# Performance work log

Measured on AMD Instinct MI355X. Metric: run time of the kernel, lower is better.

Reference implementation:

```python
import jax, jax.numpy as jnp
import numpy as np

B, DIM, H, W = 2, 384, 256, 256
HID = DIM * 1          # ffn_expansion_factor = 1 (required for source code to be consistent)
P = 8                  # patch_size


def setup_inputs() -> dict:
    key = jax.random.key(0)
    k0, k1, k2, k3, k4 = jax.random.split(key, 5)
    x = jax.random.normal(k0, (B, DIM, H, W), jnp.float32)
    # learned spectral filter: (hidden, P, P//2+1), real-valued, multiplies rfft2 coeffs
    fft_filter = jax.random.normal(k1, (HID, P, P // 2 + 1), jnp.float32)
    # project_in: 1x1 conv dim->hidden, weight (out,in)
    w_in = jax.random.normal(k2, (HID, DIM), jnp.float32) * (1.0 / np.sqrt(DIM))
    # depthwise 3x3 conv, groups=channels, weight (C,1,3,3)
    w_dw = jax.random.normal(k3, (HID, 1, 3, 3), jnp.float32) * (1.0 / 3.0)
    # project_out: 1x1 conv hidden//2 -> dim
    w_out = jax.random.normal(k4, (DIM, HID // 2), jnp.float32) * (1.0 / np.sqrt(HID // 2))
    return {"x": x, "fft_filter": fft_filter, "w_in": w_in, "w_dw": w_dw, "w_out": w_out}


def reference(x, fft_filter, w_in, w_dw, w_out):
    b, c, h, w = x.shape
    hid = w_in.shape[0]
    hb, wb = h // P, w // P
    # project_in (1x1 conv == channel GEMM)
    t = jnp.einsum('bchw,oc->bohw', x, w_in)
    # patchify into 8x8 blocks and apply per-patch 2D real FFT spectral filter.
    # reshape b c (hb p1) (wb p2) -> b c hb p1 wb p2; FFT over axes (3,5).
    tp = t.reshape(b, hid, hb, P, wb, P)
    tf = jnp.fft.rfft2(tp, axes=(3, 5))                 # (b,hid,hb,P,wb,P//2+1) complex
    tf = tf * fft_filter[None, :, None, :, None, :]
    tp = jnp.fft.irfft2(tf, s=(P, P), axes=(3, 5))
    t = tp.reshape(b, hid, h, w)
    # depthwise 3x3 conv, stride 1, padding 1
    t = jax.lax.conv_general_dilated(
        t, w_dw, window_strides=(1, 1), padding='SAME',
        feature_group_count=hid,
        dimension_numbers=('NCHW', 'OIHW', 'NCHW'))
    # gated GELU (exact erf gelu, matching torch F.gelu default)
    x1, x2 = t[:, : hid // 2], t[:, hid // 2:]
    g = jax.nn.gelu(x1, approximate=False) * x2
    # project_out (1x1 conv)
    return jnp.einsum('bchw,oc->bohw', g, w_out)
```

## Files before the change

kernel.cpp:

```cpp
#include <hip/hip_runtime.h>
#include <hip/hip_bf16.h>
#include <math.h>

#define BB 2
#define DIM 384
#define HID 384
#define HW 65536

typedef short s16x8 __attribute__((ext_vector_type(8)));
typedef short s16x4 __attribute__((ext_vector_type(4)));
typedef __bf16 bf16x8 __attribute__((ext_vector_type(8)));
typedef float f32x4 __attribute__((ext_vector_type(4)));

__device__ inline short f2b(float f) {
    __hip_bfloat16 h = __float2bfloat16(f);
    return __builtin_bit_cast(short, h);
}
__device__ inline float b2f(short s) {
    return __bfloat162float(__builtin_bit_cast(__hip_bfloat16, s));
}

__device__ inline void gl_lds16(const short* g, short* l) {
    __builtin_amdgcn_global_load_lds(
        (const __attribute__((address_space(1))) unsigned int*)g,
        (__attribute__((address_space(3))) unsigned int*)l, 16, 0, 0);
}

__global__ void k_prep(const float* __restrict__ w_in, const float* __restrict__ w_out,
                       const float* __restrict__ F,
                       short* __restrict__ wbin, short* __restrict__ wbout,
                       float* __restrict__ Dt, short* __restrict__ Rb) {
    int i = blockIdx.x * 256 + threadIdx.x;
    if (i < 147456) { wbin[i] = f2b(w_in[i]); return; }
    i -= 147456;
    if (i < 73728) { wbout[i] = f2b(w_out[i]); return; }
    i -= 73728;
    if (i < 24576) {
        int c = i >> 6, j = i & 63;
        int a = j >> 3, q = j & 7;
        float d;
        if (q >= 1 && q <= 3)
            d = F[c * 40 + a * 5 + q];
        else if (q >= 5)
            d = F[c * 40 + ((8 - a) & 7) * 5 + (8 - q)];
        else
            d = 0.5f * (F[c * 40 + a * 5 + q] + F[c * 40 + ((8 - a) & 7) * 5 + q]);
        Dt[j * 384 + c] = d * (1.f / 64.f);
        return;
    }
    i -= 24576;
    if (i < 4096) {
        int j = i >> 6, k = i & 63;
        const float cas[8] = {1.f, 1.41421356237f, 1.f, 0.f, -1.f, -1.41421356237f, -1.f, 0.f};
        int t = ((j >> 3) * (k >> 3) + (j & 7) * (k & 7)) & 7;
        Rb[i] = f2b(cas[t]);
    }
}

__global__ __launch_bounds__(256) void k_cvtx(const float* __restrict__ X, short* __restrict__ Xt) {
    int hw0 = blockIdx.x * 64, c0 = blockIdx.y * 64, b = blockIdx.z;
    __shared__ __align__(16) short S[64 * 64];
    int t = threadIdx.x;
    const float* Xb = X + ((size_t)(b * DIM) << 16);
    short* Xtb = Xt + (size_t)b * HW * DIM;
#pragma unroll
    for (int p = 0; p < 2; ++p) {
        int row = p * 32 + (t >> 3), sb = t & 7;
        const float* src = &Xb[((size_t)(c0 + row) << 16) + hw0 + sb * 8];
        float4 a = *(const float4*)src;
        float4 bq = *(const float4*)(src + 4);
        s16x8 v;
        v[0] = f2b(a.x);  v[1] = f2b(a.y);  v[2] = f2b(a.z);  v[3] = f2b(a.w);
        v[4] = f2b(bq.x); v[5] = f2b(bq.y); v[6] = f2b(bq.z); v[7] = f2b(bq.w);
        *(s16x8*)&S[row * 64 + ((sb ^ (row >> 3)) << 3)] = v;
    }
    __syncthreads();
#pragma unroll
    for (int p = 0; p < 2; ++p) {
        int row = p * 32 + (t >> 3), ch = t & 7;
        s16x8 v;
#pragma unroll
        for (int j = 0; j < 8; ++j)
            v[j] = S[(ch * 8 + j) * 64 + (row ^ (ch << 3))];
        *(s16x8*)&Xtb[(size_t)(hw0 + row) * DIM + c0 + ch * 8] = v;
    }
}

__global__ __launch_bounds__(256) void k_gemm1c(const short* __restrict__ A,
                                                const short* __restrict__ Bt,
                                                const short* __restrict__ Rb,
                                                const float* __restrict__ Dt,
                                                short* __restrict__ T) {
    __shared__ __align__(16) short SH[17408 + 4096];
    short* As = SH;
    short* Bs = SH + 4096;
    short* Rs = SH + 17408;
    int d = blockIdx.x;
    int wg = (d & 7) * 192 + (d >> 3);
    int m0 = (wg % 3) * 128;
    int tx = wg / 3;
    int h0 = (tx >> 4) * 8;
    int w0 = (tx & 15) * 16;
    int b  = blockIdx.z;
    const short* Bz = Bt + (size_t)b * HW * DIM;
    int tid = threadIdx.x;
    int lane = tid & 63, w = tid >> 6;
    int wr = w >> 1, wc = w & 1;
    int lm = lane & 15, quad = lane >> 4;

    {
        int j0 = tid >> 3, kb0 = tid & 7;
        gl_lds16(Rb + j0 * 64 + ((kb0 ^ (j0 & 7)) << 3), Rs + tid * 8);
        int t2 = tid + 256;
        int j1 = t2 >> 3, kb1 = t2 & 7;
        gl_lds16(Rb + j1 * 64 + ((kb1 ^ (j1 & 7)) << 3), Rs + t2 * 8);
    }

    f32x4 acc[4][4];
#pragma unroll
    for (int i = 0; i < 4; ++i)
#pragma unroll
        for (int j = 0; j < 4; ++j) acc[i][j] = 0.f;

    int srow = tid >> 2, sseg = tid & 3;
    int pu = srow >> 3, pv = srow & 7;
    int p1 = ((h0 + pu) << 8) + w0 + pv;
    int p2 = p1 + 8;
    for (int k0 = 0; k0 < DIM; k0 += 32) {
        gl_lds16(A + (size_t)(m0 + srow) * DIM + k0 + sseg * 8, As + tid * 8);
        gl_lds16(A + (size_t)(m0 + 64 + srow) * DIM + k0 + sseg * 8, As + (tid + 256) * 8);
        gl_lds16(Bz + (size_t)p1 * DIM + k0 + sseg * 8, Bs + tid * 8);
        gl_lds16(Bz + (size_t)p2 * DIM + k0 + sseg * 8, Bs + (tid + 256) * 8);
        __syncthreads();
        bf16x8 af[4], bfr[4];
#pragma unroll
        for (int i = 0; i < 4; ++i)
            af[i] = __builtin_bit_cast(bf16x8, *(const s16x8*)&As[(wr * 64 + i * 16 + lm) * 32 + quad * 8]);
#pragma unroll
        for (int j = 0; j < 4; ++j)
            bfr[j] = __builtin_bit_cast(bf16x8, *(const s16x8*)&Bs[(wc * 64 + j * 16 + lm) * 32 + quad * 8]);
#pragma unroll
        for (int i = 0; i < 4; ++i)
#pragma unroll
            for (int j = 0; j < 4; ++j)
                acc[i][j] = __builtin_amdgcn_mfma_f32_16x16x32_bf16(af[i], bfr[j], acc[i][j], 0, 0, 0);
        __syncthreads();
    }
#pragma unroll
    for (int i = 0; i < 4; ++i)
#pragma unroll
        for (int j = 0; j < 4; ++j)
#pragma unroll
            for (int r = 0; r < 4; ++r)
                SH[(wr * 64 + i * 16 + quad * 4 + r) * 136 + wc * 64 + j * 16 + lm] =
                    f2b(acc[i][j][r]);

    f32x4 acc2[4][4];
#pragma unroll
    for (int i = 0; i < 4; ++i)
#pragma unroll
        for (int j = 0; j < 4; ++j) acc2[i][j] = 0.f;
#pragma unroll
    for (int ks = 0; ks < 2; ++ks) {
        bf16x8 af[4], bfr[4];
#pragma unroll
        for (int i = 0; i < 4; ++i)
            af[i] = __builtin_bit_cast(bf16x8,
                *(const s16x8*)&SH[(wr * 64 + i * 16 + lm) * 136 + wc * 64 + ks * 32 + quad * 8]);
#pragma unroll
        for (int jf = 0; jf < 4; ++jf)
            bfr[jf] = __builtin_bit_cast(bf16x8,
                *(const s16x8*)&Rs[(jf * 16 + lm) * 64 + (((ks * 4 + quad) ^ (lm & 7)) << 3)]);
#pragma unroll
        for (int i = 0; i < 4; ++i)
#pragma unroll
            for (int jf = 0; jf < 4; ++jf)
                acc2[i][jf] = __builtin_amdgcn_mfma_f32_16x16x32_bf16(af[i], bfr[jf], acc2[i][jf], 0, 0, 0);
    }
#pragma unroll
    for (int i = 0; i < 4; ++i)
#pragma unroll
        for (int jf = 0; jf < 4; ++jf) {
            int j = jf * 16 + lm;
            float4 dv = *(const float4*)&Dt[j * 384 + m0 + wr * 64 + i * 16 + quad * 4];
            acc2[i][jf][0] *= dv.x; acc2[i][jf][1] *= dv.y;
            acc2[i][jf][2] *= dv.z; acc2[i][jf][3] *= dv.w;
        }
#pragma unroll
    for (int i = 0; i < 4; ++i)
#pragma unroll
        for (int jf = 0; jf < 4; ++jf)
#pragma unroll
            for (int r = 0; r < 4; ++r)
                SH[(wr * 64 + i * 16 + quad * 4 + r) * 136 + wc * 64 + jf * 16 + lm] =
                    f2b(acc2[i][jf][r]);

    f32x4 acc3[4][4];
#pragma unroll
    for (int i = 0; i < 4; ++i)
#pragma unroll
        for (int j = 0; j < 4; ++j) acc3[i][j] = 0.f;
#pragma unroll
    for (int ks = 0; ks < 2; ++ks) {
        bf16x8 af[4], bfr[4];
#pragma unroll
        for (int i = 0; i < 4; ++i)
            af[i] = __builtin_bit_cast(bf16x8,
                *(const s16x8*)&SH[(wr * 64 + i * 16 + lm) * 136 + wc * 64 + ks * 32 + quad * 8]);
#pragma unroll
        for (int uf = 0; uf < 4; ++uf)
            bfr[uf] = __builtin_bit_cast(bf16x8,
                *(const s16x8*)&Rs[(uf * 16 + lm) * 64 + (((ks * 4 + quad) ^ (lm & 7)) << 3)]);
#pragma unroll
        for (int i = 0; i < 4; ++i)
#pragma unroll
            for (int uf = 0; uf < 4; ++uf)
                acc3[i][uf] = __builtin_amdgcn_mfma_f32_16x16x32_bf16(af[i], bfr[uf], acc3[i][uf], 0, 0, 0);
    }
#pragma unroll
    for (int i = 0; i < 4; ++i)
#pragma unroll
        for (int uf = 0; uf < 4; ++uf)
#pragma unroll
            for (int r = 0; r < 4; ++r)
                SH[(wr * 64 + i * 16 + quad * 4 + r) * 136 + wc * 64 + uf * 16 + lm] =
                    f2b(acc3[i][uf][r]);
    __syncthreads();
    int pid0 = (h0 >> 3) * 32 + (w0 >> 3);
#pragma unroll
    for (int kq = 0; kq < 8; ++kq) {
        int idx = kq * 256 + tid;
        int row = idx >> 4, seg = idx & 15;
        s16x8 vv = *(const s16x8*)&SH[row * 136 + seg * 8];
        *(s16x8*)&T[(((size_t)(b * HID + m0 + row)) << 16) + (pid0 << 6) + seg * 8] = vv;
    }
}

__global__ __launch_bounds__(256) void k_dwgt(const short* __restrict__ Y,
                                              const float* __restrict__ Wdw,
                                              short* __restrict__ Gt) {
    int bz = blockIdx.z;
    int b  = bz / 24;
    int cg = bz % 24;
    int c0 = cg * 8;
    int h0 = blockIdx.y * 16, w0 = blockIdx.x * 64;
    __shared__ __align__(16) short S[16][18][80];
    __shared__ float sw[16][9];
    int tid = threadIdx.x;
    if (tid < 144) {
        int p = tid / 9, j = tid % 9;
        int ch = (p < 8) ? (c0 + p) : (c0 + p - 8 + 192);
        sw[p][j] = Wdw[ch * 9 + j];
    }
    for (int t = tid; t < 2880; t += 256) {
        int v = t % 10, r = (t / 10) % 18, p = t / 180;
        int gh = h0 + r - 1;
        int gw = w0 + v * 8 - 8;
        int ch = (p < 8) ? (c0 + p) : (c0 + p - 8 + 192);
        s16x8 val = {0, 0, 0, 0, 0, 0, 0, 0};
        if (gh >= 0 && gh < 256 && gw >= 0 && gw <= 248) {
            int pid = ((gh >> 3) << 5) + (gw >> 3);
            val = *(const s16x8*)&Y[((size_t)(b * HID + ch) << 16) + (pid << 6) + ((gh & 7) << 3)];
        }
        *(s16x8*)&S[p][r][v * 8] = val;
    }
    __syncthreads();
    s16x8 ov[4];
#pragma unroll
    for (int it = 0; it < 4; ++it) {
        int idx = it * 256 + tid;
        int p = idx >> 7, run = idx & 127;
        int r = run >> 3, c8 = (run & 7) * 8;
        float z1[8], z2[8];
#pragma unroll
        for (int k = 0; k < 8; ++k) { z1[k] = 0.f; z2[k] = 0.f; }
#pragma unroll
        for (int i = 0; i < 3; ++i) {
            {
                s16x4 wv[4];
#pragma unroll
                for (int q = 0; q < 4; ++q) wv[q] = *(const s16x4*)&S[p][r + i][c8 + 4 + q * 4];
                float fv[10];
#pragma unroll
                for (int q = 0; q < 10; ++q) fv[q] = b2f(wv[(q + 3) >> 2][(q + 3) & 3]);
#pragma unroll
                for (int j = 0; j < 3; ++j) {
                    float wgt = sw[p][i * 3 + j];
#pragma unroll
                    for (int k = 0; k < 8; ++k) z1[k] += fv[k + j] * wgt;
                }
            }
            {
                s16x4 wv[4];
#pragma unroll
                for (int q = 0; q < 4; ++q) wv[q] = *(const s16x4*)&S[p + 8][r + i][c8 + 4 + q * 4];
                float fv[10];
#pragma unroll
                for (int q = 0; q < 10; ++q) fv[q] = b2f(wv[(q + 3) >> 2][(q + 3) & 3]);
#pragma unroll
                for (int j = 0; j < 3; ++j) {
                    float wgt = sw[p + 8][i * 3 + j];
#pragma unroll
                    for (int k = 0; k < 8; ++k) z2[k] += fv[k + j] * wgt;
                }
            }
        }
#pragma unroll
        for (int k = 0; k < 8; ++k) {
            float g = 0.5f * z1[k] * (1.f + erff(z1[k] * 0.70710678118654752f));
            ov[it][k] = f2b(g * z2[k]);
        }
    }
    __syncthreads();
    short* Ob = (short*)S;
#pragma unroll
    for (int it = 0; it < 4; ++it) {
        int idx = it * 256 + tid;
        int p = idx >> 7, run = idx & 127;
        int pos = (run >> 3) * 64 + (run & 7) * 8;
#pragma unroll
        for (int k = 0; k < 8; ++k)
            Ob[(pos + k) * 9 + p] = ov[it][k];
    }
    __syncthreads();
    short* Gb = Gt + (((size_t)(b * 24 + cg)) << 16) * 8;
#pragma unroll
    for (int it = 0; it < 4; ++it) {
        int pos = it * 256 + tid;
        int r = pos >> 6, cl = pos & 63;
        s16x8 v;
#pragma unroll
        for (int k = 0; k < 8; ++k) v[k] = Ob[pos * 9 + k];
        *(s16x8*)&Gb[(size_t)(((h0 + r) << 8) + w0 + cl) * 8] = v;
    }
}

__global__ __launch_bounds__(256) void k_gemm_bf16(const short* __restrict__ A,
                                                   const short* __restrict__ Bt,
                                                   float* __restrict__ C,
                                                   int N, int K) {
    __shared__ __align__(16) short As[128 * 32];
    __shared__ __align__(16) short Bs[128 * 32];
    const short* Bz = Bt + (size_t)blockIdx.z * (size_t)N * K;
    float* Cz = C + (size_t)blockIdx.z * (size_t)384 * N;
    int d = blockIdx.x;
    int wg = (d & 7) * 192 + (d >> 3);
    int m0 = (wg % 3) * 128;
    int n0 = (wg / 3) * 128;
    int tid = threadIdx.x;
    int lane = tid & 63, w = tid >> 6;
    int wr = w >> 1, wc = w & 1;
    int lm = lane & 15, quad = lane >> 4;

    f32x4 acc[4][4];
#pragma unroll
    for (int i = 0; i < 4; ++i)
#pragma unroll
        for (int j = 0; j < 4; ++j) acc[i][j] = 0.f;

    int srow = tid >> 2, sseg = tid & 3;
    for (int k0 = 0; k0 < K; k0 += 32) {
        gl_lds16(A + (size_t)(m0 + srow) * K + k0 + sseg * 8, As + tid * 8);
        gl_lds16(A + (size_t)(m0 + 64 + srow) * K + k0 + sseg * 8, As + (tid + 256) * 8);
        gl_lds16(Bz + ((size_t)((k0 >> 3) + sseg) * HW + n0 + srow) * 8, Bs + tid * 8);
        gl_lds16(Bz + ((size_t)((k0 >> 3) + sseg) * HW + n0 + 64 + srow) * 8, Bs + (tid + 256) * 8);
        __syncthreads();
        bf16x8 af[4], bfr[4];
#pragma unroll
        for (int i = 0; i < 4; ++i)
            af[i] = __builtin_bit_cast(bf16x8, *(const s16x8*)&As[(wr * 64 + i * 16 + lm) * 32 + quad * 8]);
#pragma unroll
        for (int j = 0; j < 4; ++j)
            bfr[j] = __builtin_bit_cast(bf16x8, *(const s16x8*)&Bs[(wc * 64 + j * 16 + lm) * 32 + quad * 8]);
#pragma unroll
        for (int i = 0; i < 4; ++i)
#pragma unroll
            for (int j = 0; j < 4; ++j)
                acc[i][j] = __builtin_amdgcn_mfma_f32_16x16x32_bf16(af[i], bfr[j], acc[i][j], 0, 0, 0);
        __syncthreads();
    }
#pragma unroll
    for (int i = 0; i < 4; ++i) {
        int r0 = m0 + wr * 64 + i * 16 + quad * 4;
#pragma unroll
        for (int j = 0; j < 4; ++j) {
            int cidx = n0 + wc * 64 + j * 16 + lm;
#pragma unroll
            for (int r = 0; r < 4; ++r)
                Cz[(size_t)(r0 + r) * N + cidx] = acc[i][j][r];
        }
    }
}

extern "C" void kernel_launch(void* const* d_in, const int* in_sizes, int n_in,
                              void* d_out, int out_size, void* d_ws, size_t ws_size,
                              hipStream_t stream) {
    const float* x     = (const float*)d_in[0];
    const float* ff    = (const float*)d_in[1];
    const float* w_in  = (const float*)d_in[2];
    const float* w_dw  = (const float*)d_in[3];
    const float* w_out = (const float*)d_in[4];
    float* out = (float*)d_out;

    char* ws = (char*)d_ws;
    float* Dt   = (float*)ws;
    short* wbin = (short*)(ws + 98304);
    short* wbout = (short*)(ws + 393216);
    short* Rbuf = (short*)(ws + 540672);
    short* bufA = (short*)(ws + 548864);
    short* bufB = (short*)(ws + 548864 + (size_t)100663296);
    short* Gt = bufA;

    k_prep<<<976, 256, 0, stream>>>(w_in, w_out, ff, wbin, wbout, Dt, Rbuf);
    k_cvtx<<<dim3(HW / 64, DIM / 64, BB), 256, 0, stream>>>(x, bufA);

    k_gemm1c<<<dim3(1536, 1, BB), 256, 0, stream>>>(wbin, bufA, Rbuf, Dt, bufB);

    k_dwgt<<<dim3(4, 16, BB * 24), 256, 0, stream>>>(bufB, w_dw, Gt);

    k_gemm_bf16<<<dim3(1536, 1, BB), 256, 0, stream>>>(wbout, Gt, out, HW, 192);
}
```

Before: 585.7 us.

## Fuse fp32-to-bf16 input conversion into first GEMM and double-buffer both GEMMs

```diff
diff --git a/kernel.cpp b/kernel.cpp
--- a/kernel.cpp
+++ b/kernel.cpp
@@ -57,43 +57,12 @@
     }
 }
 
-__global__ __launch_bounds__(256) void k_cvtx(const float* __restrict__ X, short* __restrict__ Xt) {
-    int hw0 = blockIdx.x * 64, c0 = blockIdx.y * 64, b = blockIdx.z;
-    __shared__ __align__(16) short S[64 * 64];
-    int t = threadIdx.x;
-    const float* Xb = X + ((size_t)(b * DIM) << 16);
-    short* Xtb = Xt + (size_t)b * HW * DIM;
-#pragma unroll
-    for (int p = 0; p < 2; ++p) {
-        int row = p * 32 + (t >> 3), sb = t & 7;
-        const float* src = &Xb[((size_t)(c0 + row) << 16) + hw0 + sb * 8];
-        float4 a = *(const float4*)src;
-        float4 bq = *(const float4*)(src + 4);
-        s16x8 v;
-        v[0] = f2b(a.x);  v[1] = f2b(a.y);  v[2] = f2b(a.z);  v[3] = f2b(a.w);
-        v[4] = f2b(bq.x); v[5] = f2b(bq.y); v[6] = f2b(bq.z); v[7] = f2b(bq.w);
-        *(s16x8*)&S[row * 64 + ((sb ^ (row >> 3)) << 3)] = v;
-    }
-    __syncthreads();
-#pragma unroll
-    for (int p = 0; p < 2; ++p) {
-        int row = p * 32 + (t >> 3), ch = t & 7;
-        s16x8 v;
-#pragma unroll
-        for (int j = 0; j < 8; ++j)
-            v[j] = S[(ch * 8 + j) * 64 + (row ^ (ch << 3))];
-        *(s16x8*)&Xtb[(size_t)(hw0 + row) * DIM + c0 + ch * 8] = v;
-    }
-}
-
 __global__ __launch_bounds__(256) void k_gemm1c(const short* __restrict__ A,
-                                                const short* __restrict__ Bt,
+                                                const float* __restrict__ X,
                                                 const short* __restrict__ Rb,
                                                 const float* __restrict__ Dt,
                                                 short* __restrict__ T) {
     __shared__ __align__(16) short SH[17408 + 4096];
-    short* As = SH;
-    short* Bs = SH + 4096;
     short* Rs = SH + 17408;
     int d = blockIdx.x;
     int wg = (d & 7) * 192 + (d >> 3);
@@ -102,7 +71,6 @@
     int h0 = (tx >> 4) * 8;
     int w0 = (tx & 15) * 16;
     int b  = blockIdx.z;
-    const short* Bz = Bt + (size_t)b * HW * DIM;
     int tid = threadIdx.x;
     int lane = tid & 63, w = tid >> 6;
     int wr = w >> 1, wc = w & 1;
@@ -116,36 +84,70 @@
         gl_lds16(Rb + j1 * 64 + ((kb1 ^ (j1 & 7)) << 3), Rs + t2 * 8);
     }
 
+    int srow = tid >> 2, sseg = tid & 3;
+    int cB = tid & 31, uB = tid >> 5;
+    const float* xp = X + (((size_t)(b * DIM + cB)) << 16) + ((h0 + uB) << 8) + w0;
+    int bwb = uB * 256 + cB;
+
     f32x4 acc[4][4];
 #pragma unroll
     for (int i = 0; i < 4; ++i)
 #pragma unroll
         for (int j = 0; j < 4; ++j) acc[i][j] = 0.f;
 
-    int srow = tid >> 2, sseg = tid & 3;
-    int pu = srow >> 3, pv = srow & 7;
-    int p1 = ((h0 + pu) << 8) + w0 + pv;
-    int p2 = p1 + 8;
-    for (int k0 = 0; k0 < DIM; k0 += 32) {
-        gl_lds16(A + (size_t)(m0 + srow) * DIM + k0 + sseg * 8, As + tid * 8);
-        gl_lds16(A + (size_t)(m0 + 64 + srow) * DIM + k0 + sseg * 8, As + (tid + 256) * 8);
-        gl_lds16(Bz + (size_t)p1 * DIM + k0 + sseg * 8, Bs + tid * 8);
-        gl_lds16(Bz + (size_t)p2 * DIM + k0 + sseg * 8, Bs + (tid + 256) * 8);
+    float4 rB[4];
+#pragma unroll
+    for (int q = 0; q < 4; ++q) rB[q] = ((const float4*)xp)[q];
+    gl_lds16(A + (size_t)(m0 + srow) * DIM + sseg * 8, SH + tid * 8);
+    gl_lds16(A + (size_t)(m0 + 64 + srow) * DIM + sseg * 8, SH + (tid + 256) * 8);
+    {
+        short* p = SH + 4096 + bwb;
+        p[0]    = f2b(rB[0].x); p[32]   = f2b(rB[0].y); p[64]   = f2b(rB[0].z); p[96]   = f2b(rB[0].w);
+        p[128]  = f2b(rB[1].x); p[160]  = f2b(rB[1].y); p[192]  = f2b(rB[1].z); p[224]  = f2b(rB[1].w);
+        p[2048] = f2b(rB[2].x); p[2080] = f2b(rB[2].y); p[2112] = f2b(rB[2].z); p[2144] = f2b(rB[2].w);
+        p[2176] = f2b(rB[3].x); p[2208] = f2b(rB[3].y); p[2240] = f2b(rB[3].z); p[2272] = f2b(rB[3].w);
+    }
+    __syncthreads();
+
+    int cur = 0;
+#pragma unroll 2
+    for (int kc = 0; kc < 12; ++kc) {
+        short* nA = SH + ((cur ^ 1) ? 8192 : 0);
+        short* nB = SH + ((cur ^ 1) ? 12288 : 4096);
+        if (kc < 11) {
+            const float* xq = xp + ((size_t)(kc + 1) << 21);
+#pragma unroll
+            for (int q = 0; q < 4; ++q) rB[q] = ((const float4*)xq)[q];
+            gl_lds16(A + (size_t)(m0 + srow) * DIM + (kc + 1) * 32 + sseg * 8, nA + tid * 8);
+            gl_lds16(A + (size_t)(m0 + 64 + srow) * DIM + (kc + 1) * 32 + sseg * 8, nA + (tid + 256) * 8);
+        }
+        {
+            const short* Ar = SH + (cur ? 8192 : 0);
+            const short* Br = SH + (cur ? 12288 : 4096);
+            bf16x8 af[4], bfr[4];
+#pragma unroll
+            for (int i = 0; i < 4; ++i)
+                af[i] = __builtin_bit_cast(bf16x8, *(const s16x8*)&Ar[(wr * 64 + i * 16 + lm) * 32 + quad * 8]);
+#pragma unroll
+            for (int j = 0; j < 4; ++j)
+                bfr[j] = __builtin_bit_cast(bf16x8, *(const s16x8*)&Br[(wc * 64 + j * 16 + lm) * 32 + quad * 8]);
+#pragma unroll
+            for (int i = 0; i < 4; ++i)
+#pragma unroll
+                for (int j = 0; j < 4; ++j)
+                    acc[i][j] = __builtin_amdgcn_mfma_f32_16x16x32_bf16(af[i], bfr[j], acc[i][j], 0, 0, 0);
+        }
+        if (kc < 11) {
+            short* p = nB + bwb;
+            p[0]    = f2b(rB[0].x); p[32]   = f2b(rB[0].y); p[64]   = f2b(rB[0].z); p[96]   = f2b(rB[0].w);
+            p[128]  = f2b(rB[1].x); p[160]  = f2b(rB[1].y); p[192]  = f2b(rB[1].z); p[224]  = f2b(rB[1].w);
+            p[2048] = f2b(rB[2].x); p[2080] = f2b(rB[2].y); p[2112] = f2b(rB[2].z); p[2144] = f2b(rB[2].w);
+            p[2176] = f2b(rB[3].x); p[2208] = f2b(rB[3].y); p[2240] = f2b(rB[3].z); p[2272] = f2b(rB[3].w);
+        }
         __syncthreads();
-        bf16x8 af[4], bfr[4];
-#pragma unroll
-        for (int i = 0; i < 4; ++i)
-            af[i] = __builtin_bit_cast(bf16x8, *(const s16x8*)&As[(wr * 64 + i * 16 + lm) * 32 + quad * 8]);
-#pragma unroll
-        for (int j = 0; j < 4; ++j)
-            bfr[j] = __builtin_bit_cast(bf16x8, *(const s16x8*)&Bs[(wc * 64 + j * 16 + lm) * 32 + quad * 8]);
-#pragma unroll
-        for (int i = 0; i < 4; ++i)
-#pragma unroll
-            for (int j = 0; j < 4; ++j)
-                acc[i][j] = __builtin_amdgcn_mfma_f32_16x16x32_bf16(af[i], bfr[j], acc[i][j], 0, 0, 0);
-        __syncthreads();
-    }
+        cur ^= 1;
+    }
+
 #pragma unroll
     for (int i = 0; i < 4; ++i)
 #pragma unroll
@@ -339,8 +341,7 @@
                                                    const short* __restrict__ Bt,
                                                    float* __restrict__ C,
                                                    int N, int K) {
-    __shared__ __align__(16) short As[128 * 32];
-    __shared__ __align__(16) short Bs[128 * 32];
+    __shared__ __align__(16) short SH[16384];
     const short* Bz = Bt + (size_t)blockIdx.z * (size_t)N * K;
     float* Cz = C + (size_t)blockIdx.z * (size_t)384 * N;
     int d = blockIdx.x;
@@ -359,25 +360,40 @@
         for (int j = 0; j < 4; ++j) acc[i][j] = 0.f;
 
     int srow = tid >> 2, sseg = tid & 3;
-    for (int k0 = 0; k0 < K; k0 += 32) {
-        gl_lds16(A + (size_t)(m0 + srow) * K + k0 + sseg * 8, As + tid * 8);
-        gl_lds16(A + (size_t)(m0 + 64 + srow) * K + k0 + sseg * 8, As + (tid + 256) * 8);
-        gl_lds16(Bz + ((size_t)((k0 >> 3) + sseg) * HW + n0 + srow) * 8, Bs + tid * 8);
-        gl_lds16(Bz + ((size_t)((k0 >> 3) + sseg) * HW + n0 + 64 + srow) * 8, Bs + (tid + 256) * 8);
-        __syncthreads();
+    gl_lds16(A + (size_t)(m0 + srow) * K + sseg * 8, SH + tid * 8);
+    gl_lds16(A + (size_t)(m0 + 64 + srow) * K + sseg * 8, SH + (tid + 256) * 8);
+    gl_lds16(Bz + ((size_t)sseg * HW + n0 + srow) * 8, SH + 4096 + tid * 8);
+    gl_lds16(Bz + ((size_t)sseg * HW + n0 + 64 + srow) * 8, SH + 4096 + (tid + 256) * 8);
+    __syncthreads();
+
+    int cur = 0;
+#pragma unroll 2
+    for (int kc = 0; kc < 6; ++kc) {
+        if (kc < 5) {
+            short* nA = SH + ((cur ^ 1) ? 8192 : 0);
+            short* nB = nA + 4096;
+            int k0 = (kc + 1) * 32;
+            gl_lds16(A + (size_t)(m0 + srow) * K + k0 + sseg * 8, nA + tid * 8);
+            gl_lds16(A + (size_t)(m0 + 64 + srow) * K + k0 + sseg * 8, nA + (tid + 256) * 8);
+            gl_lds16(Bz + ((size_t)((k0 >> 3) + sseg) * HW + n0 + srow) * 8, nB + tid * 8);
+            gl_lds16(Bz + ((size_t)((k0 >> 3) + sseg) * HW + n0 + 64 + srow) * 8, nB + (tid + 256) * 8);
+        }
+        const short* Ar = SH + (cur ? 8192 : 0);
+        const short* Br = Ar + 4096;
         bf16x8 af[4], bfr[4];
 #pragma unroll
         for (int i = 0; i < 4; ++i)
-            af[i] = __builtin_bit_cast(bf16x8, *(const s16x8*)&As[(wr * 64 + i * 16 + lm) * 32 + quad * 8]);
+            af[i] = __builtin_bit_cast(bf16x8, *(const s16x8*)&Ar[(wr * 64 + i * 16 + lm) * 32 + quad * 8]);
 #pragma unroll
         for (int j = 0; j < 4; ++j)
-            bfr[j] = __builtin_bit_cast(bf16x8, *(const s16x8*)&Bs[(wc * 64 + j * 16 + lm) * 32 + quad * 8]);
+            bfr[j] = __builtin_bit_cast(bf16x8, *(const s16x8*)&Br[(wc * 64 + j * 16 + lm) * 32 + quad * 8]);
 #pragma unroll
         for (int i = 0; i < 4; ++i)
 #pragma unroll
             for (int j = 0; j < 4; ++j)
                 acc[i][j] = __builtin_amdgcn_mfma_f32_16x16x32_bf16(af[i], bfr[j], acc[i][j], 0, 0, 0);
         __syncthreads();
+        cur ^= 1;
     }
 #pragma unroll
     for (int i = 0; i < 4; ++i) {
@@ -407,16 +423,14 @@
     short* wbin = (short*)(ws + 98304);
     short* wbout = (short*)(ws + 393216);
     short* Rbuf = (short*)(ws + 540672);
-    short* bufA = (short*)(ws + 548864);
-    short* bufB = (short*)(ws + 548864 + (size_t)100663296);
-    short* Gt = bufA;
+    short* Gt   = (short*)(ws + 548864);
+    short* Tbuf = (short*)(ws + 548864 + (size_t)100663296);
 
     k_prep<<<976, 256, 0, stream>>>(w_in, w_out, ff, wbin, wbout, Dt, Rbuf);
-    k_cvtx<<<dim3(HW / 64, DIM / 64, BB), 256, 0, stream>>>(x, bufA);
-
-    k_gemm1c<<<dim3(1536, 1, BB), 256, 0, stream>>>(wbin, bufA, Rbuf, Dt, bufB);
-
-    k_dwgt<<<dim3(4, 16, BB * 24), 256, 0, stream>>>(bufB, w_dw, Gt);
+
+    k_gemm1c<<<dim3(1536, 1, BB), 256, 0, stream>>>(wbin, x, Rbuf, Dt, Tbuf);
+
+    k_dwgt<<<dim3(4, 16, BB * 24), 256, 0, stream>>>(Tbuf, w_dw, Gt);
 
     k_gemm_bf16<<<dim3(1536, 1, BB), 256, 0, stream>>>(wbout, Gt, out, HW, 192);
 }
```

Result: faster. 572.6 us (-2.2%).

## Store X in patch-major order and deepen GEMM K-chunks with swizzled LDS

Applied to the files above, without the earlier changes.

```diff
diff --git a/kernel.cpp b/kernel.cpp
--- a/kernel.cpp
+++ b/kernel.cpp
@@ -29,7 +29,7 @@
 __global__ void k_prep(const float* __restrict__ w_in, const float* __restrict__ w_out,
                        const float* __restrict__ F,
                        short* __restrict__ wbin, short* __restrict__ wbout,
-                       float* __restrict__ Dt, short* __restrict__ Rb) {
+                       float* __restrict__ Dtc, short* __restrict__ Rb) {
     int i = blockIdx.x * 256 + threadIdx.x;
     if (i < 147456) { wbin[i] = f2b(w_in[i]); return; }
     i -= 147456;
@@ -45,7 +45,7 @@
             d = F[c * 40 + ((8 - a) & 7) * 5 + (8 - q)];
         else
             d = 0.5f * (F[c * 40 + a * 5 + q] + F[c * 40 + ((8 - a) & 7) * 5 + q]);
-        Dt[j * 384 + c] = d * (1.f / 64.f);
+        Dtc[i] = d * (1.f / 64.f);
         return;
     }
     i -= 24576;
@@ -75,6 +75,7 @@
         *(s16x8*)&S[row * 64 + ((sb ^ (row >> 3)) << 3)] = v;
     }
     __syncthreads();
+    int h = hw0 >> 8, wb0 = hw0 & 255;
 #pragma unroll
     for (int p = 0; p < 2; ++p) {
         int row = p * 32 + (t >> 3), ch = t & 7;
@@ -82,27 +83,27 @@
 #pragma unroll
         for (int j = 0; j < 8; ++j)
             v[j] = S[(ch * 8 + j) * 64 + (row ^ (ch << 3))];
-        *(s16x8*)&Xtb[(size_t)(hw0 + row) * DIM + c0 + ch * 8] = v;
-    }
-}
-
-__global__ __launch_bounds__(256) void k_gemm1c(const short* __restrict__ A,
-                                                const short* __restrict__ Bt,
+        int wv = wb0 + row;
+        int rowp = (((h >> 3) << 5) + (wv >> 3)) * 64 + ((h & 7) << 3) + (wv & 7);
+        *(s16x8*)&Xtb[(size_t)rowp * DIM + c0 + ch * 8] = v;
+    }
+}
+
+__global__ __launch_bounds__(256) void k_gemm1c(const short* __restrict__ W,
+                                                const short* __restrict__ Xt,
                                                 const short* __restrict__ Rb,
-                                                const float* __restrict__ Dt,
+                                                const float* __restrict__ Dtc,
                                                 short* __restrict__ T) {
     __shared__ __align__(16) short SH[17408 + 4096];
-    short* As = SH;
-    short* Bs = SH + 4096;
+    short* Xs = SH;
+    short* Ws = SH + 8192;
     short* Rs = SH + 17408;
     int d = blockIdx.x;
     int wg = (d & 7) * 192 + (d >> 3);
     int m0 = (wg % 3) * 128;
     int tx = wg / 3;
-    int h0 = (tx >> 4) * 8;
-    int w0 = (tx & 15) * 16;
+    int pid0 = tx * 2;
     int b  = blockIdx.z;
-    const short* Bz = Bt + (size_t)b * HW * DIM;
     int tid = threadIdx.x;
     int lane = tid & 63, w = tid >> 6;
     int wr = w >> 1, wc = w & 1;
@@ -116,123 +117,127 @@
         gl_lds16(Rb + j1 * 64 + ((kb1 ^ (j1 & 7)) << 3), Rs + t2 * 8);
     }
 
+    const short* Xbase = Xt + ((size_t)b * HW + (size_t)pid0 * 64) * DIM;
+
     f32x4 acc[4][4];
 #pragma unroll
     for (int i = 0; i < 4; ++i)
 #pragma unroll
         for (int j = 0; j < 4; ++j) acc[i][j] = 0.f;
 
-    int srow = tid >> 2, sseg = tid & 3;
-    int pu = srow >> 3, pv = srow & 7;
-    int p1 = ((h0 + pu) << 8) + w0 + pv;
-    int p2 = p1 + 8;
-    for (int k0 = 0; k0 < DIM; k0 += 32) {
-        gl_lds16(A + (size_t)(m0 + srow) * DIM + k0 + sseg * 8, As + tid * 8);
-        gl_lds16(A + (size_t)(m0 + 64 + srow) * DIM + k0 + sseg * 8, As + (tid + 256) * 8);
-        gl_lds16(Bz + (size_t)p1 * DIM + k0 + sseg * 8, Bs + tid * 8);
-        gl_lds16(Bz + (size_t)p2 * DIM + k0 + sseg * 8, Bs + (tid + 256) * 8);
+    for (int kc = 0; kc < 6; ++kc) {
+        int k0 = kc * 64;
+#pragma unroll
+        for (int q = 0; q < 4; ++q) {
+            int G = q * 256 + tid;
+            int row = G >> 3;
+            int lg = ((G & 7) ^ (row & 7)) << 3;
+            gl_lds16(Xbase + (size_t)row * DIM + k0 + lg, Xs + G * 8);
+            gl_lds16(W + (size_t)(m0 + row) * DIM + k0 + lg, Ws + G * 8);
+        }
         __syncthreads();
+#pragma unroll
+        for (int ks = 0; ks < 2; ++ks) {
+            int csw = (((ks * 4 + quad) ^ (lm & 7)) << 3);
+            bf16x8 af[4], bfr[4];
+#pragma unroll
+            for (int i = 0; i < 4; ++i)
+                af[i] = __builtin_bit_cast(bf16x8, *(const s16x8*)&Xs[(wr * 64 + i * 16 + lm) * 64 + csw]);
+#pragma unroll
+            for (int j = 0; j < 4; ++j)
+                bfr[j] = __builtin_bit_cast(bf16x8, *(const s16x8*)&Ws[(wc * 64 + j * 16 + lm) * 64 + csw]);
+#pragma unroll
+            for (int i = 0; i < 4; ++i)
+#pragma unroll
+                for (int j = 0; j < 4; ++j)
+                    acc[i][j] = __builtin_amdgcn_mfma_f32_16x16x32_bf16(af[i], bfr[j], acc[i][j], 0, 0, 0);
+        }
+        __syncthreads();
+    }
+
+#pragma unroll
+    for (int i = 0; i < 4; ++i)
+#pragma unroll
+        for (int j = 0; j < 4; ++j) {
+            s16x4 v4;
+#pragma unroll
+            for (int r = 0; r < 4; ++r) v4[r] = f2b(acc[i][j][r]);
+            *(s16x4*)&SH[(wc * 64 + j * 16 + lm) * 136 + wr * 64 + i * 16 + quad * 4] = v4;
+        }
+
+    f32x4 acc2[4][4];
+#pragma unroll
+    for (int i = 0; i < 4; ++i)
+#pragma unroll
+        for (int j = 0; j < 4; ++j) acc2[i][j] = 0.f;
+#pragma unroll
+    for (int ks = 0; ks < 2; ++ks) {
+        int csw = (((ks * 4 + quad) ^ (lm & 7)) << 3);
         bf16x8 af[4], bfr[4];
 #pragma unroll
         for (int i = 0; i < 4; ++i)
-            af[i] = __builtin_bit_cast(bf16x8, *(const s16x8*)&As[(wr * 64 + i * 16 + lm) * 32 + quad * 8]);
+            af[i] = __builtin_bit_cast(bf16x8, *(const s16x8*)&Rs[(i * 16 + lm) * 64 + csw]);
 #pragma unroll
         for (int j = 0; j < 4; ++j)
-            bfr[j] = __builtin_bit_cast(bf16x8, *(const s16x8*)&Bs[(wc * 64 + j * 16 + lm) * 32 + quad * 8]);
+            bfr[j] = __builtin_bit_cast(bf16x8,
+                *(const s16x8*)&SH[(wc * 64 + j * 16 + lm) * 136 + wr * 64 + ks * 32 + quad * 8]);
 #pragma unroll
         for (int i = 0; i < 4; ++i)
 #pragma unroll
             for (int j = 0; j < 4; ++j)
-                acc[i][j] = __builtin_amdgcn_mfma_f32_16x16x32_bf16(af[i], bfr[j], acc[i][j], 0, 0, 0);
-        __syncthreads();
-    }
-#pragma unroll
-    for (int i = 0; i < 4; ++i)
+                acc2[i][j] = __builtin_amdgcn_mfma_f32_16x16x32_bf16(af[i], bfr[j], acc2[i][j], 0, 0, 0);
+    }
+#pragma unroll
+    for (int i = 0; i < 4; ++i)
+#pragma unroll
+        for (int j2 = 0; j2 < 4; ++j2) {
+            float4 dv = *(const float4*)&Dtc[(size_t)(m0 + wc * 64 + j2 * 16 + lm) * 64 + i * 16 + quad * 4];
+            s16x4 v4;
+            v4[0] = f2b(acc2[i][j2][0] * dv.x);
+            v4[1] = f2b(acc2[i][j2][1] * dv.y);
+            v4[2] = f2b(acc2[i][j2][2] * dv.z);
+            v4[3] = f2b(acc2[i][j2][3] * dv.w);
+            *(s16x4*)&SH[(wc * 64 + j2 * 16 + lm) * 136 + wr * 64 + i * 16 + quad * 4] = v4;
+        }
+
+    f32x4 acc3[4][4];
+#pragma unroll
+    for (int i = 0; i < 4; ++i)
+#pragma unroll
+        for (int j = 0; j < 4; ++j) acc3[i][j] = 0.f;
+#pragma unroll
+    for (int ks = 0; ks < 2; ++ks) {
+        int csw = (((ks * 4 + quad) ^ (lm & 7)) << 3);
+        bf16x8 af[4], bfr[4];
+#pragma unroll
+        for (int i = 0; i < 4; ++i)
+            af[i] = __builtin_bit_cast(bf16x8, *(const s16x8*)&Rs[(i * 16 + lm) * 64 + csw]);
 #pragma unroll
         for (int j = 0; j < 4; ++j)
-#pragma unroll
-            for (int r = 0; r < 4; ++r)
-                SH[(wr * 64 + i * 16 + quad * 4 + r) * 136 + wc * 64 + j * 16 + lm] =
-                    f2b(acc[i][j][r]);
-
-    f32x4 acc2[4][4];
-#pragma unroll
-    for (int i = 0; i < 4; ++i)
-#pragma unroll
-        for (int j = 0; j < 4; ++j) acc2[i][j] = 0.f;
-#pragma unroll
-    for (int ks = 0; ks < 2; ++ks) {
-        bf16x8 af[4], bfr[4];
+            bfr[j] = __builtin_bit_cast(bf16x8,
+                *(const s16x8*)&SH[(wc * 64 + j * 16 + lm) * 136 + wr * 64 + ks * 32 + quad * 8]);
 #pragma unroll
         for (int i = 0; i < 4; ++i)
-            af[i] = __builtin_bit_cast(bf16x8,
-                *(const s16x8*)&SH[(wr * 64 + i * 16 + lm) * 136 + wc * 64 + ks * 32 + quad * 8]);
-#pragma unroll
-        for (int jf = 0; jf < 4; ++jf)
-            bfr[jf] = __builtin_bit_cast(bf16x8,
-                *(const s16x8*)&Rs[(jf * 16 + lm) * 64 + (((ks * 4 + quad) ^ (lm & 7)) << 3)]);
-#pragma unroll
-        for (int i = 0; i < 4; ++i)
-#pragma unroll
-            for (int jf = 0; jf < 4; ++jf)
-                acc2[i][jf] = __builtin_amdgcn_mfma_f32_16x16x32_bf16(af[i], bfr[jf], acc2[i][jf], 0, 0, 0);
-    }
-#pragma unroll
-    for (int i = 0; i < 4; ++i)
-#pragma unroll
-        for (int jf = 0; jf < 4; ++jf) {
-            int j = jf * 16 + lm;
-            float4 dv = *(const float4*)&Dt[j * 384 + m0 + wr * 64 + i * 16 + quad * 4];
-            acc2[i][jf][0] *= dv.x; acc2[i][jf][1] *= dv.y;
-            acc2[i][jf][2] *= dv.z; acc2[i][jf][3] *= dv.w;
-        }
-#pragma unroll
-    for (int i = 0; i < 4; ++i)
-#pragma unroll
-        for (int jf = 0; jf < 4; ++jf)
-#pragma unroll
-            for (int r = 0; r < 4; ++r)
-                SH[(wr * 64 + i * 16 + quad * 4 + r) * 136 + wc * 64 + jf * 16 + lm] =
-                    f2b(acc2[i][jf][r]);
-
-    f32x4 acc3[4][4];
-#pragma unroll
-    for (int i = 0; i < 4; ++i)
-#pragma unroll
-        for (int j = 0; j < 4; ++j) acc3[i][j] = 0.f;
-#pragma unroll
-    for (int ks = 0; ks < 2; ++ks) {
-        bf16x8 af[4], bfr[4];
-#pragma unroll
-        for (int i = 0; i < 4; ++i)
-            af[i] = __builtin_bit_cast(bf16x8,
-                *(const s16x8*)&SH[(wr * 64 + i * 16 + lm) * 136 + wc * 64 + ks * 32 + quad * 8]);
-#pragma unroll
-        for (int uf = 0; uf < 4; ++uf)
-            bfr[uf] = __builtin_bit_cast(bf16x8,
-                *(const s16x8*)&Rs[(uf * 16 + lm) * 64 + (((ks * 4 + quad) ^ (lm & 7)) << 3)]);
-#pragma unroll
-        for (int i = 0; i < 4; ++i)
-#pragma unroll
-            for (int uf = 0; uf < 4; ++uf)
-                acc3[i][uf] = __builtin_amdgcn_mfma_f32_16x16x32_bf16(af[i], bfr[uf], acc3[i][uf], 0, 0, 0);
-    }
-#pragma unroll
-    for (int i = 0; i < 4; ++i)
-#pragma unroll
-        for (int uf = 0; uf < 4; ++uf)
-#pragma unroll
-            for (int r = 0; r < 4; ++r)
-                SH[(wr * 64 + i * 16 + quad * 4 + r) * 136 + wc * 64 + uf * 16 + lm] =
-                    f2b(acc3[i][uf][r]);
+#pragma unroll
+            for (int j = 0; j < 4; ++j)
+                acc3[i][j] = __builtin_amdgcn_mfma_f32_16x16x32_bf16(af[i], bfr[j], acc3[i][j], 0, 0, 0);
+    }
+#pragma unroll
+    for (int i = 0; i < 4; ++i)
+#pragma unroll
+        for (int j2 = 0; j2 < 4; ++j2) {
+            s16x4 v4;
+#pragma unroll
+            for (int r = 0; r < 4; ++r) v4[r] = f2b(acc3[i][j2][r]);
+            *(s16x4*)&SH[(wc * 64 + j2 * 16 + lm) * 136 + wr * 64 + i * 16 + quad * 4] = v4;
+        }
     __syncthreads();
-    int pid0 = (h0 >> 3) * 32 + (w0 >> 3);
 #pragma unroll
     for (int kq = 0; kq < 8; ++kq) {
         int idx = kq * 256 + tid;
         int row = idx >> 4, seg = idx & 15;
         s16x8 vv = *(const s16x8*)&SH[row * 136 + seg * 8];
-        *(s16x8*)&T[(((size_t)(b * HID + m0 + row)) << 16) + (pid0 << 6) + seg * 8] = vv;
+        *(s16x8*)&T[(((size_t)(b * HID + m0 + row)) << 16) + pid0 * 64 + seg * 8] = vv;
     }
 }
 
@@ -339,8 +344,7 @@
                                                    const short* __restrict__ Bt,
                                                    float* __restrict__ C,
                                                    int N, int K) {
-    __shared__ __align__(16) short As[128 * 32];
-    __shared__ __align__(16) short Bs[128 * 32];
+    __shared__ __align__(16) short SH[16384];
     const short* Bz = Bt + (size_t)blockIdx.z * (size_t)N * K;
     float* Cz = C + (size_t)blockIdx.z * (size_t)384 * N;
     int d = blockIdx.x;
@@ -358,25 +362,33 @@
 #pragma unroll
         for (int j = 0; j < 4; ++j) acc[i][j] = 0.f;
 
-    int srow = tid >> 2, sseg = tid & 3;
-    for (int k0 = 0; k0 < K; k0 += 32) {
-        gl_lds16(A + (size_t)(m0 + srow) * K + k0 + sseg * 8, As + tid * 8);
-        gl_lds16(A + (size_t)(m0 + 64 + srow) * K + k0 + sseg * 8, As + (tid + 256) * 8);
-        gl_lds16(Bz + ((size_t)((k0 >> 3) + sseg) * HW + n0 + srow) * 8, Bs + tid * 8);
-        gl_lds16(Bz + ((size_t)((k0 >> 3) + sseg) * HW + n0 + 64 + srow) * 8, Bs + (tid + 256) * 8);
+    for (int kc = 0; kc < 3; ++kc) {
+        int k0 = kc * 64;
+#pragma unroll
+        for (int q = 0; q < 4; ++q) {
+            int G = q * 256 + tid;
+            int row = G >> 3;
+            int lg = (G & 7) ^ (row & 7);
+            gl_lds16(A + (size_t)(m0 + row) * K + k0 + (lg << 3), SH + G * 8);
+            gl_lds16(Bz + ((size_t)((k0 >> 3) + lg) * HW + n0 + row) * 8, SH + 8192 + G * 8);
+        }
         __syncthreads();
-        bf16x8 af[4], bfr[4];
-#pragma unroll
-        for (int i = 0; i < 4; ++i)
-            af[i] = __builtin_bit_cast(bf16x8, *(const s16x8*)&As[(wr * 64 + i * 16 + lm) * 32 + quad * 8]);
-#pragma unroll
-        for (int j = 0; j < 4; ++j)
-            bfr[j] = __builtin_bit_cast(bf16x8, *(const s16x8*)&Bs[(wc * 64 + j * 16 + lm) * 32 + quad * 8]);
-#pragma unroll
-        for (int i = 0; i < 4; ++i)
+#pragma unroll
+        for (int ks = 0; ks < 2; ++ks) {
+            int csw = (((ks * 4 + quad) ^ (lm & 7)) << 3);
+            bf16x8 af[4], bfr[4];
+#pragma unroll
+            for (int i = 0; i < 4; ++i)
+                af[i] = __builtin_bit_cast(bf16x8, *(const s16x8*)&SH[(wr * 64 + i * 16 + lm) * 64 + csw]);
 #pragma unroll
             for (int j = 0; j < 4; ++j)
-                acc[i][j] = __builtin_amdgcn_mfma_f32_16x16x32_bf16(af[i], bfr[j], acc[i][j], 0, 0, 0);
+                bfr[j] = __builtin_bit_cast(bf16x8, *(const s16x8*)&SH[8192 + (wc * 64 + j * 16 + lm) * 64 + csw]);
+#pragma unroll
+            for (int i = 0; i < 4; ++i)
+#pragma unroll
+                for (int j = 0; j < 4; ++j)
+                    acc[i][j] = __builtin_amdgcn_mfma_f32_16x16x32_bf16(af[i], bfr[j], acc[i][j], 0, 0, 0);
+        }
         __syncthreads();
     }
 #pragma unroll
@@ -403,7 +415,7 @@
     float* out = (float*)d_out;
 
     char* ws = (char*)d_ws;
-    float* Dt   = (float*)ws;
+    float* Dtc  = (float*)ws;
     short* wbin = (short*)(ws + 98304);
     short* wbout = (short*)(ws + 393216);
     short* Rbuf = (short*)(ws + 540672);
@@ -411,10 +423,11 @@
     short* bufB = (short*)(ws + 548864 + (size_t)100663296);
     short* Gt = bufA;
 
-    k_prep<<<976, 256, 0, stream>>>(w_in, w_out, ff, wbin, wbout, Dt, Rbuf);
+    k_prep<<<976, 256, 0, stream>>>(w_in, w_out, ff, wbin, wbout, Dtc, Rbuf);
+
     k_cvtx<<<dim3(HW / 64, DIM / 64, BB), 256, 0, stream>>>(x, bufA);
 
-    k_gemm1c<<<dim3(1536, 1, BB), 256, 0, stream>>>(wbin, bufA, Rbuf, Dt, bufB);
+    k_gemm1c<<<dim3(1536, 1, BB), 256, 0, stream>>>(wbin, bufA, Rbuf, Dtc, bufB);
 
     k_dwgt<<<dim3(4, 16, BB * 24), 256, 0, stream>>>(bufB, w_dw, Gt);
 
```

After: 580.2 us. Within noise of the previous version (-0.9%).
